# Kernel optimization log

Hardware: AMD Instinct MI355X
Metric: run time of the kernel (lower is better)

The kernel has to match this reference:

```python
import jax, jax.numpy as jnp
import numpy as np

# ---- Cl(3,0) Cayley table; blade order [1, e1,e2,e3, e12,e13,e23, e123] ----
def _build_cayley():
    blades = [0b000, 0b001, 0b010, 0b100, 0b011, 0b101, 0b110, 0b111]
    pos = {b: i for i, b in enumerate(blades)}
    def sign(a, b):
        s, a = 0, a >> 1
        while a:
            s += bin(a & b).count('1')
            a >>= 1
        return -1.0 if s & 1 else 1.0
    C = np.zeros((8, 8, 8), np.float32)
    for i, a in enumerate(blades):
        for k, b in enumerate(blades):
            C[i, pos[a ^ b], k] = sign(a, b)  # e_a * e_b -> sign * e_(a^b), metric all +1
    return jnp.asarray(C)

CAYLEY = _build_cayley()
EPS = 1e-6
SEQ = 25      # num_nodes (5) + num_edges (20)
HEADS = 8

def _expand_grades(w):
    # [..., 4] (per-grade) -> [..., 8] (per-blade), grade dims 1,3,3,1
    return jnp.concatenate([w[..., 0:1],
                            jnp.repeat(w[..., 1:2], 3, -1),
                            jnp.repeat(w[..., 2:3], 3, -1),
                            w[..., 3:4]], axis=-1)

def mv_linear(x, w, b):
    # x [N, in, 8], w [out, in, 4], b [out]; bias only on scalar blade
    y = jnp.einsum('nmi,omi->noi', x, _expand_grades(w))
    return y.at[..., 0].add(b)

def mv_layernorm(x, a):
    n = jnp.linalg.norm(x, axis=-1, keepdims=True)   # [N, c, 1] multivector norm
    n = jnp.mean(n, axis=1, keepdims=True) + EPS     # mean over channels -> [N, 1, 1]
    return a[None, :, None] * x / n

def mv_silu(x, a, b):
    # invariants: scalar component + squared grade magnitudes (mag2)
    inv = jnp.stack([x[..., 0],
                     jnp.sum(x[..., 1:4] ** 2, -1),
                     jnp.sum(x[..., 4:7] ** 2, -1),
                     x[..., 7] ** 2], axis=-1)       # [N, c, 4]
    return _expand_grades(jax.nn.sigmoid(a * inv + b)) * x

def geometric_product(a, b):
    return jnp.einsum('nci,ijk,nck->ncj', a, CAYLEY, b)


def setup_inputs() -> dict:
    key = jax.random.key(0)
    ks = iter(jax.random.split(key, 40))
    D, B = 128, 1024
    N = B * SEQ
    s = 0.05
    rn = lambda *sh: jax.random.normal(next(ks), sh, jnp.float32) * s
    return dict(
        src=jax.random.normal(next(ks), (N, D, 8), jnp.float32),
        ln1_a=jnp.ones(D, jnp.float32), ln2_a=jnp.ones(D, jnp.float32), ln3_a=jnp.ones(D, jnp.float32),
        wq=rn(D, D, 4), bq=jnp.zeros(D, jnp.float32),
        wk=rn(D, D, 4), bk=jnp.zeros(D, jnp.float32),
        wv=rn(D, D, 4), bv=jnp.zeros(D, jnp.float32),
        wo=rn(D, D, 4), bo=jnp.zeros(D, jnp.float32),
        gw1=rn(2 * D, D, 4), gb1=jnp.zeros(2 * D, jnp.float32),
        gw2=rn(2 * D, D, 4), gb2=jnp.zeros(2 * D, jnp.float32),
        gw3=rn(D, 2 * D, 4), gb3=jnp.zeros(D, jnp.float32),
        gna=jnp.ones(D, jnp.float32),
        mw1=rn(2 * D, D, 4), mb1=jnp.zeros(2 * D, jnp.float32),
        sa=jnp.ones((2 * D, 4), jnp.float32), sb=jnp.zeros((2 * D, 4), jnp.float32),
        mw2=rn(D, 2 * D, 4), mb2=jnp.zeros(D, jnp.float32),
    )


def reference(src, ln1_a, ln2_a, ln3_a, wq, bq, wk, bk, wv, bv, wo, bo,
              gw1, gb1, gw2, gb2, gw3, gb3, gna,
              mw1, mb1, sa, sb, mw2, mb2):
    N, D, _ = src.shape
    B, dh = N // SEQ, D // HEADS

    def attention(x):
        q = mv_linear(x, wq, bq).reshape(B, SEQ, HEADS, dh, 8)
        k = mv_linear(x, wk, bk).reshape(B, SEQ, HEADS, dh, 8)
        v = mv_linear(x, wv, bv).reshape(B, SEQ, HEADS, dh, 8)
        scores = jnp.einsum('bshdi,bthdi->bhst', q, k) / np.float32(np.sqrt(dh * 8))
        p = jax.nn.softmax(scores, axis=-1)
        o = jnp.einsum('bhst,bthdi->bshdi', p, v).reshape(N, D, 8)
        return mv_linear(o, wo, bo)

    # pre-norm attention + residual
    x = src + attention(mv_layernorm(src, ln1_a))
    x = mv_layernorm(x, ln2_a)
    # GP_Layer: two grade-wise linears -> geometric product -> linear -> norm
    xl = mv_linear(x, gw1, gb1)
    xr = mv_linear(x, gw2, gb2)
    g = mv_layernorm(mv_linear(geometric_product(xl, xr), gw3, gb3), gna)
    x = x + g
    x = mv_layernorm(x, ln3_a)
    # gated MLP: MVLinear -> MVSiLU -> MVLinear
    ff = mv_linear(mv_silu(mv_linear(x, mw1, mb1), sa, sb), mw2, mb2)
    return x + ff
```

## Files before the change

### kernel.cpp

```cpp
#include <hip/hip_runtime.h>
#include <hip/hip_bf16.h>
#include <math.h>

#define NROWS 25600
#define SEQL  25
#define EPSV  1e-6f

typedef __hip_bfloat16 bf16;
typedef __attribute__((ext_vector_type(4))) float f32x4;
typedef __attribute__((ext_vector_type(8))) short bf16x8;
typedef __attribute__((ext_vector_type(4))) short s16x4;
typedef unsigned int u32;

#define GLD16(gp_, lp_) __builtin_amdgcn_global_load_lds( \
    (const __attribute__((address_space(1))) u32*)(gp_), \
    (__attribute__((address_space(3))) u32*)(lp_), 16, 0, 0)

__device__ __forceinline__ float b2f(short s) {
  return __uint_as_float(((u32)(unsigned short)s) << 16);
}
__device__ __forceinline__ short f2b(float f) {
  __hip_bfloat16 h = __float2bfloat16(f);
  return *reinterpret_cast<short*>(&h);
}

__device__ __forceinline__ void gprod(const float* a, const float* b, float* r) {
  const int M[8] = {0,1,2,4,3,5,6,7};
  const int P[8] = {0,1,2,4,3,5,6,7};
#pragma unroll
  for (int i = 0; i < 8; ++i) {
    const int ma = M[i];
#pragma unroll
    for (int k = 0; k < 8; ++k) {
      const int mb = M[k];
      int par = 0;
      for (int t = ma >> 1; t; t >>= 1) par += __popc(t & mb);
      const float s = (par & 1) ? -1.f : 1.f;
      r[P[ma ^ mb]] += s * a[i] * b[k];
    }
  }
}

template<int KT, int ON>
__global__ __launch_bounds__(256) void gemm_kernel(
    const bf16* __restrict__ A, const bf16* __restrict__ W,
    const float* __restrict__ bias, const float* __restrict__ invnm,
    bf16* __restrict__ Y)
{
  __shared__ __align__(16) short As[128 * 128];
  __shared__ __align__(16) short Bs[128 * 128];
  const int tid  = threadIdx.x;
  const int lane = tid & 63;
  const int wid  = tid >> 6;
  const int pl   = blockIdx.z;
  const int g    = (pl == 0) ? 0 : ((pl < 4) ? 1 : ((pl < 7) ? 2 : 3));
  const size_t n0 = (size_t)blockIdx.x * 128;
  const int c0    = blockIdx.y * 128;
  const bf16* Ab = A + (size_t)pl * NROWS * KT + n0 * KT;
  const bf16* Wb = W + ((size_t)g * ON + c0) * KT;

  f32x4 acc[4][4];
#pragma unroll
  for (int i = 0; i < 4; ++i)
#pragma unroll
    for (int j = 0; j < 4; ++j) acc[i][j] = (f32x4){0.f, 0.f, 0.f, 0.f};

  const int wm = (wid & 1) * 64;
  const int wn = (wid >> 1) * 64;
  const int lg  = lane >> 4;
  const int c8  = lane & 15;
  const int l15 = lane & 15;

  constexpr int NC = KT / 128;
#pragma unroll
  for (int kc = 0; kc < NC; ++kc) {
#pragma unroll
    for (int j = 0; j < 8; ++j) {
      const int row = wid * 32 + j * 4 + lg;
      const int sw = (c8 ^ (row & 7)) * 8;
      const bf16* ga = Ab + (size_t)row * KT + kc * 128 + sw;
      const bf16* gb = Wb + (size_t)row * KT + kc * 128 + sw;
      GLD16(ga, &As[wid * 4096 + j * 512]);
      GLD16(gb, &Bs[wid * 4096 + j * 512]);
    }
    __syncthreads();
#pragma unroll
    for (int ks = 0; ks < 4; ++ks) {
      bf16x8 af[4], bg[4];
#pragma unroll
      for (int i = 0; i < 4; ++i) {
        const int rA = wm + i * 16 + l15;
        const int rB = wn + i * 16 + l15;
        af[i] = *(const bf16x8*)&As[rA * 128 + (((ks * 4 + lg) ^ (rA & 7)) * 8)];
        bg[i] = *(const bf16x8*)&Bs[rB * 128 + (((ks * 4 + lg) ^ (rB & 7)) * 8)];
      }
#pragma unroll
      for (int mi = 0; mi < 4; ++mi)
#pragma unroll
        for (int ni = 0; ni < 4; ++ni)
          acc[mi][ni] = __builtin_amdgcn_mfma_f32_16x16x32_bf16(af[mi], bg[ni], acc[mi][ni], 0, 0, 0);
    }
    if (kc + 1 < NC) __syncthreads();
  }

  const int cr = (lane >> 4) * 4;
  const int cc = lane & 15;
  bf16* Yb = Y + (size_t)pl * NROWS * ON;
#pragma unroll
  for (int mi = 0; mi < 4; ++mi) {
#pragma unroll
    for (int j = 0; j < 4; ++j) {
      const size_t n = n0 + wm + mi * 16 + cr + j;
      const float sc = invnm ? invnm[n] : 1.f;
#pragma unroll
      for (int ni = 0; ni < 4; ++ni) {
        const int colg = c0 + wn + ni * 16 + cc;
        float v = acc[mi][ni][j] * sc;
        if (pl == 0) v += bias[colg];
        Yb[n * ON + colg] = __float2bfloat16(v);
      }
    }
  }
}

__global__ __launch_bounds__(256) void wprep_all_kernel(
    const float* wq, const float* wk, const float* wv, const float* wo,
    const float* gw1, const float* gw2, const float* gw3,
    const float* mw1, const float* mw2,
    const float* ln1, const float* ln2, const float* ln3,
    bf16* WQ, bf16* WK, bf16* WV, bf16* WO,
    bf16* WG1, bf16* WG2, bf16* WG3, bf16* WM1, bf16* WM2)
{
  const int gid = blockIdx.x * 256 + threadIdx.x;
  const float* w; const float* ln; bf16* out; int K; int idx; int sz;
  if      (gid <  16384) { w=wq;  ln=ln1;     out=WQ;  K=128; idx=gid;          sz=16384; }
  else if (gid <  32768) { w=wk;  ln=ln1;     out=WK;  K=128; idx=gid-16384;    sz=16384; }
  else if (gid <  49152) { w=wv;  ln=ln1;     out=WV;  K=128; idx=gid-32768;    sz=16384; }
  else if (gid <  65536) { w=wo;  ln=nullptr; out=WO;  K=128; idx=gid-49152;    sz=16384; }
  else if (gid <  98304) { w=gw1; ln=ln2;     out=WG1; K=128; idx=gid-65536;    sz=32768; }
  else if (gid < 131072) { w=gw2; ln=ln2;     out=WG2; K=128; idx=gid-98304;    sz=32768; }
  else if (gid < 163840) { w=gw3; ln=nullptr; out=WG3; K=256; idx=gid-131072;   sz=32768; }
  else if (gid < 196608) { w=mw1; ln=ln3;     out=WM1; K=128; idx=gid-163840;   sz=32768; }
  else                   { w=mw2; ln=nullptr; out=WM2; K=256; idx=gid-196608;   sz=32768; }
  const int k = idx % K;
  const float s = ln ? ln[k] : 1.f;
  const float4 wv4 = *(const float4*)(w + (size_t)idx * 4);
  out[0 * sz + idx] = __float2bfloat16(wv4.x * s);
  out[1 * sz + idx] = __float2bfloat16(wv4.y * s);
  out[2 * sz + idx] = __float2bfloat16(wv4.z * s);
  out[3 * sz + idx] = __float2bfloat16(wv4.w * s);
}

__global__ __launch_bounds__(256) void repack_kernel(
    const float* __restrict__ src, bf16* __restrict__ Xp, float* __restrict__ nminv)
{
  const int tid = threadIdx.x;
  const size_t base = ((size_t)blockIdx.x * 256 + tid) * 4;
  const size_t P = (size_t)NROWS * 128;
  float v[4][8];
  const float4* sp = (const float4*)(src + base * 8);
  float part = 0.f;
#pragma unroll
  for (int e = 0; e < 4; ++e) {
    const float4 a = sp[e * 2], b = sp[e * 2 + 1];
    v[e][0]=a.x; v[e][1]=a.y; v[e][2]=a.z; v[e][3]=a.w;
    v[e][4]=b.x; v[e][5]=b.y; v[e][6]=b.z; v[e][7]=b.w;
    float ss = 0.f;
#pragma unroll
    for (int p = 0; p < 8; ++p) ss += v[e][p] * v[e][p];
    part += sqrtf(ss);
  }
#pragma unroll
  for (int p = 0; p < 8; ++p) {
    s16x4 o;
#pragma unroll
    for (int e = 0; e < 4; ++e) o[e] = f2b(v[e][p]);
    *(s16x4*)(Xp + p * P + base) = o;
  }
#pragma unroll
  for (int off = 1; off < 32; off <<= 1) part += __shfl_xor(part, off);
  if ((tid & 31) == 0) nminv[base >> 7] = 1.f / (part / 128.f + EPSV);
}

__global__ __launch_bounds__(256) void attn_kernel(
    bf16* __restrict__ Q, const bf16* __restrict__ K, const bf16* __restrict__ V)
{
  __shared__ float Pld[4][32 * 36];
  const int tid  = threadIdx.x;
  const int lane = tid & 63;
  const int wid  = tid >> 6;
  const int job  = blockIdx.x * 4 + wid;
  const int b    = job >> 3;
  const int h    = job & 7;
  const size_t PS = (size_t)NROWS * 128;
  const int rowbase = b * SEQL;
  const int l15 = lane & 15;
  const int lg  = lane >> 4;

  f32x4 acc[2][2];
#pragma unroll
  for (int si = 0; si < 2; ++si)
#pragma unroll
    for (int ti = 0; ti < 2; ++ti) acc[si][ti] = (f32x4){0.f,0.f,0.f,0.f};

#pragma unroll
  for (int ks = 0; ks < 4; ++ks) {
    const int f = ks * 32 + lg * 8;
    const int p = f >> 4, d = f & 15;
    bf16x8 aq[2], bk[2];
#pragma unroll
    for (int si = 0; si < 2; ++si) {
      int s = si * 16 + l15; if (s > 24) s = 24;
      aq[si] = *(const bf16x8*)(Q + (size_t)p * PS + (size_t)(rowbase + s) * 128 + h * 16 + d);
    }
#pragma unroll
    for (int ti = 0; ti < 2; ++ti) {
      int t = ti * 16 + l15; if (t > 24) t = 24;
      bk[ti] = *(const bf16x8*)(K + (size_t)p * PS + (size_t)(rowbase + t) * 128 + h * 16 + d);
    }
#pragma unroll
    for (int si = 0; si < 2; ++si)
#pragma unroll
      for (int ti = 0; ti < 2; ++ti)
        acc[si][ti] = __builtin_amdgcn_mfma_f32_16x16x32_bf16(aq[si], bk[ti], acc[si][ti], 0, 0, 0);
  }

  const float scale = 0.08838834764831845f;
  float pv[2][2][4];
#pragma unroll
  for (int si = 0; si < 2; ++si)
#pragma unroll
    for (int ti = 0; ti < 2; ++ti)
#pragma unroll
      for (int r = 0; r < 4; ++r) {
        float v = acc[si][ti][r] * scale;
        if (ti * 16 + l15 > 24) v = -1e30f;
        pv[si][ti][r] = v;
      }
#pragma unroll
  for (int si = 0; si < 2; ++si)
#pragma unroll
    for (int r = 0; r < 4; ++r) {
      float m = fmaxf(pv[si][0][r], pv[si][1][r]);
#pragma unroll
      for (int off = 1; off < 16; off <<= 1) m = fmaxf(m, __shfl_xor(m, off));
      const float e0 = __expf(pv[si][0][r] - m);
      const float e1 = __expf(pv[si][1][r] - m);
      float sum = e0 + e1;
#pragma unroll
      for (int off = 1; off < 16; off <<= 1) sum += __shfl_xor(sum, off);
      const float inv = 1.f / sum;
      pv[si][0][r] = e0 * inv;
      pv[si][1][r] = e1 * inv;
    }

  float* Pw = &Pld[wid][0];
#pragma unroll
  for (int si = 0; si < 2; ++si)
#pragma unroll
    for (int ti = 0; ti < 2; ++ti)
#pragma unroll
      for (int r = 0; r < 4; ++r)
        Pw[(si * 16 + lg * 4 + r) * 36 + ti * 16 + l15] = pv[si][ti][r];
  __syncthreads();

  const int p2 = lane >> 3;
  const int d2 = (lane & 7) * 2;
  const bf16* vb = V + (size_t)p2 * PS + (size_t)rowbase * 128 + h * 16 + d2;
  float vlo[32], vhi[32];
#pragma unroll
  for (int t = 0; t < SEQL; ++t) {
    const __hip_bfloat162 vv = *(const __hip_bfloat162*)(vb + (size_t)t * 128);
    vlo[t] = __bfloat162float(vv.x);
    vhi[t] = __bfloat162float(vv.y);
  }
#pragma unroll
  for (int t = SEQL; t < 32; ++t) { vlo[t] = 0.f; vhi[t] = 0.f; }

  bf16* ob = Q + (size_t)p2 * PS + (size_t)rowbase * 128 + h * 16 + d2;
  for (int s = 0; s < SEQL; ++s) {
    const float4* pr = reinterpret_cast<const float4*>(&Pld[wid][s * 36]);
    float a0 = 0.f, a1 = 0.f;
#pragma unroll
    for (int t4 = 0; t4 < 8; ++t4) {
      const float4 pq = pr[t4];
      a0 += pq.x * vlo[t4*4+0] + pq.y * vlo[t4*4+1] + pq.z * vlo[t4*4+2] + pq.w * vlo[t4*4+3];
      a1 += pq.x * vhi[t4*4+0] + pq.y * vhi[t4*4+1] + pq.z * vhi[t4*4+2] + pq.w * vhi[t4*4+3];
    }
    __hip_bfloat162 o2;
    o2.x = __float2bfloat16(a0);
    o2.y = __float2bfloat16(a1);
    *(__hip_bfloat162*)(ob + (size_t)s * 128) = o2;
  }
}

__global__ __launch_bounds__(256) void xres_kernel(
    const float* __restrict__ src, const bf16* __restrict__ AO,
    bf16* __restrict__ X, float* __restrict__ nminv)
{
  const int tid = threadIdx.x;
  const size_t base = ((size_t)blockIdx.x * 256 + tid) * 4;
  const size_t P = (size_t)NROWS * 128;
  float v[4][8];
  const float4* sp = (const float4*)(src + base * 8);
#pragma unroll
  for (int e = 0; e < 4; ++e) {
    const float4 a = sp[e * 2], b = sp[e * 2 + 1];
    v[e][0]=a.x; v[e][1]=a.y; v[e][2]=a.z; v[e][3]=a.w;
    v[e][4]=b.x; v[e][5]=b.y; v[e][6]=b.z; v[e][7]=b.w;
  }
  float part = 0.f;
  float ss[4] = {0.f, 0.f, 0.f, 0.f};
#pragma unroll
  for (int p = 0; p < 8; ++p) {
    const s16x4 av = *(const s16x4*)(AO + p * P + base);
    s16x4 o;
#pragma unroll
    for (int e = 0; e < 4; ++e) {
      v[e][p] += b2f(av[e]);
      o[e] = f2b(v[e][p]);
      ss[e] += v[e][p] * v[e][p];
    }
    *(s16x4*)(X + p * P + base) = o;
  }
#pragma unroll
  for (int e = 0; e < 4; ++e) part += sqrtf(ss[e]);
#pragma unroll
  for (int off = 1; off < 32; off <<= 1) part += __shfl_xor(part, off);
  if ((tid & 31) == 0) nminv[base >> 7] = 1.f / (part / 128.f + EPSV);
}

__global__ __launch_bounds__(256) void gp_kernel(
    bf16* __restrict__ XL, const bf16* __restrict__ XR)
{
  const size_t base = ((size_t)blockIdx.x * 256 + threadIdx.x) * 4;
  const size_t P = (size_t)NROWS * 256;
  s16x4 av[8], bv[8], rv[8];
#pragma unroll
  for (int p = 0; p < 8; ++p) {
    av[p] = *(const s16x4*)(XL + p * P + base);
    bv[p] = *(const s16x4*)(XR + p * P + base);
  }
#pragma unroll
  for (int e = 0; e < 4; ++e) {
    float a[8], b[8], r[8] = {0.f,0.f,0.f,0.f,0.f,0.f,0.f,0.f};
#pragma unroll
    for (int p = 0; p < 8; ++p) { a[p] = b2f(av[p][e]); b[p] = b2f(bv[p][e]); }
    gprod(a, b, r);
#pragma unroll
    for (int p = 0; p < 8; ++p) rv[p][e] = f2b(r[p]);
  }
#pragma unroll
  for (int p = 0; p < 8; ++p) *(s16x4*)(XL + p * P + base) = rv[p];
}

__global__ __launch_bounds__(256) void combine_kernel(
    bf16* __restrict__ X, const bf16* __restrict__ Gl,
    const float* __restrict__ ln2a, const float* __restrict__ gna,
    const float* __restrict__ nm2inv, float* __restrict__ nm4inv)
{
  const int tid = threadIdx.x;
  const size_t base = ((size_t)blockIdx.x * 256 + tid) * 4;
  const size_t P = (size_t)NROWS * 128;
  const size_t n = base >> 7;
  const int c = (int)(base & 127);

  float gv[4][8];
  float ssg[4] = {0.f,0.f,0.f,0.f};
#pragma unroll
  for (int p = 0; p < 8; ++p) {
    const s16x4 g4 = *(const s16x4*)(Gl + p * P + base);
#pragma unroll
    for (int e = 0; e < 4; ++e) { gv[e][p] = b2f(g4[e]); ssg[e] += gv[e][p] * gv[e][p]; }
  }
  float partg = sqrtf(ssg[0]) + sqrtf(ssg[1]) + sqrtf(ssg[2]) + sqrtf(ssg[3]);
#pragma unroll
  for (int off = 1; off < 32; off <<= 1) partg += __shfl_xor(partg, off);
  const float invg = 1.f / (partg / 128.f + EPSV);

  const float n2 = nm2inv[n];
  float s2[4], sg[4];
#pragma unroll
  for (int e = 0; e < 4; ++e) { s2[e] = ln2a[c + e] * n2; sg[e] = gna[c + e] * invg; }

  float ss[4] = {0.f,0.f,0.f,0.f};
#pragma unroll
  for (int p = 0; p < 8; ++p) {
    const s16x4 x4 = *(const s16x4*)(X + p * P + base);
    s16x4 o;
#pragma unroll
    for (int e = 0; e < 4; ++e) {
      const float v = s2[e] * b2f(x4[e]) + sg[e] * gv[e][p];
      o[e] = f2b(v);
      ss[e] += v * v;
    }
    *(s16x4*)(X + p * P + base) = o;
  }
  float part = sqrtf(ss[0]) + sqrtf(ss[1]) + sqrtf(ss[2]) + sqrtf(ss[3]);
#pragma unroll
  for (int off = 1; off < 32; off <<= 1) part += __shfl_xor(part, off);
  if ((tid & 31) == 0) nm4inv[n] = 1.f / (part / 128.f + EPSV);
}

__global__ __launch_bounds__(256) void silu_kernel(
    bf16* __restrict__ H, const float* __restrict__ sa, const float* __restrict__ sb)
{
  const size_t base = ((size_t)blockIdx.x * 256 + threadIdx.x) * 4;
  const int c = (int)(base & 255);
  const size_t P = (size_t)NROWS * 256;
  s16x4 hv[8];
#pragma unroll
  for (int p = 0; p < 8; ++p) hv[p] = *(const s16x4*)(H + p * P + base);
#pragma unroll
  for (int e = 0; e < 4; ++e) {
    float v[8];
#pragma unroll
    for (int p = 0; p < 8; ++p) v[p] = b2f(hv[p][e]);
    const float i0 = v[0];
    const float i1 = v[1]*v[1] + v[2]*v[2] + v[3]*v[3];
    const float i2 = v[4]*v[4] + v[5]*v[5] + v[6]*v[6];
    const float i3 = v[7]*v[7];
    const int cc = c + e;
    const float g0 = 1.f / (1.f + __expf(-(sa[cc*4+0]*i0 + sb[cc*4+0])));
    const float g1 = 1.f / (1.f + __expf(-(sa[cc*4+1]*i1 + sb[cc*4+1])));
    const float g2 = 1.f / (1.f + __expf(-(sa[cc*4+2]*i2 + sb[cc*4+2])));
    const float g3 = 1.f / (1.f + __expf(-(sa[cc*4+3]*i3 + sb[cc*4+3])));
    v[0]*=g0; v[1]*=g1; v[2]*=g1; v[3]*=g1; v[4]*=g2; v[5]*=g2; v[6]*=g2; v[7]*=g3;
#pragma unroll
    for (int p = 0; p < 8; ++p) hv[p][e] = f2b(v[p]);
  }
#pragma unroll
  for (int p = 0; p < 8; ++p) *(s16x4*)(H + p * P + base) = hv[p];
}

__global__ __launch_bounds__(256) void final_kernel(
    const bf16* __restrict__ X3, const bf16* __restrict__ FF,
    const float* __restrict__ ln3a, const float* __restrict__ nm4inv,
    float* __restrict__ out)
{
  const size_t base = ((size_t)blockIdx.x * 256 + threadIdx.x) * 4;
  const int c = (int)(base & 127);
  const size_t n = base >> 7;
  const size_t P = (size_t)NROWS * 128;
  const float nm = nm4inv[n];
  float o[4][8];
#pragma unroll
  for (int p = 0; p < 8; ++p) {
    const s16x4 x4 = *(const s16x4*)(X3 + p * P + base);
    const s16x4 f4 = *(const s16x4*)(FF + p * P + base);
#pragma unroll
    for (int e = 0; e < 4; ++e)
      o[e][p] = ln3a[c + e] * nm * b2f(x4[e]) + b2f(f4[e]);
  }
  float4* op = (float4*)(out + base * 8);
#pragma unroll
  for (int e = 0; e < 4; ++e) {
    float4 lo, hi;
    lo.x=o[e][0]; lo.y=o[e][1]; lo.z=o[e][2]; lo.w=o[e][3];
    hi.x=o[e][4]; hi.y=o[e][5]; hi.z=o[e][6]; hi.w=o[e][7];
    op[e * 2] = lo;
    op[e * 2 + 1] = hi;
  }
}

extern "C" void kernel_launch(void* const* d_in, const int* in_sizes, int n_in,
                              void* d_out, int out_size, void* d_ws, size_t ws_size,
                              hipStream_t stream) {
  (void)in_sizes; (void)n_in; (void)out_size; (void)ws_size;
  const float* src   = (const float*)d_in[0];
  const float* ln1_a = (const float*)d_in[1];
  const float* ln2_a = (const float*)d_in[2];
  const float* ln3_a = (const float*)d_in[3];
  const float* wq = (const float*)d_in[4];  const float* bq = (const float*)d_in[5];
  const float* wk = (const float*)d_in[6];  const float* bk = (const float*)d_in[7];
  const float* wv = (const float*)d_in[8];  const float* bv = (const float*)d_in[9];
  const float* wo = (const float*)d_in[10]; const float* bo = (const float*)d_in[11];
  const float* gw1 = (const float*)d_in[12]; const float* gb1 = (const float*)d_in[13];
  const float* gw2 = (const float*)d_in[14]; const float* gb2 = (const float*)d_in[15];
  const float* gw3 = (const float*)d_in[16]; const float* gb3 = (const float*)d_in[17];
  const float* gna = (const float*)d_in[18];
  const float* mw1 = (const float*)d_in[19]; const float* mb1 = (const float*)d_in[20];
  const float* sa  = (const float*)d_in[21]; const float* sb  = (const float*)d_in[22];
  const float* mw2 = (const float*)d_in[23]; const float* mb2 = (const float*)d_in[24];

  const size_t P128 = (size_t)NROWS * 128;
  char* ws = (char*)d_ws;
  bf16* R1 = (bf16*)ws;
  bf16* R2 = (bf16*)(ws + 104857600);
  bf16* WQ = (bf16*)(ws + 157286400);
  bf16* WK = WQ + 65536;
  bf16* WV = WK + 65536;
  bf16* WO = WV + 65536;
  bf16* WG1 = WO + 65536;
  bf16* WG2 = WG1 + 131072;
  bf16* WG3 = WG2 + 131072;
  bf16* WM1 = WG3 + 131072;
  bf16* WM2 = WM1 + 131072;
  float* nm1 = (float*)(ws + 159121408);
  float* nm2 = nm1 + NROWS;
  float* nm4 = nm2 + NROWS;

  bf16* Dd = (bf16*)d_out;
  bf16* Xp = R2;
  bf16* Kp = R1;
  bf16* Vp = R1 + P128;

  wprep_all_kernel<<<896, 256, 0, stream>>>(
      wq, wk, wv, wo, gw1, gw2, gw3, mw1, mw2,
      ln1_a, ln2_a, ln3_a,
      WQ, WK, WV, WO, WG1, WG2, WG3, WM1, WM2);

  repack_kernel<<<3200, 256, 0, stream>>>(src, Xp, nm1);

  dim3 g128(NROWS / 128, 1, 8), g256(NROWS / 128, 2, 8);
  gemm_kernel<128, 128><<<g128, 256, 0, stream>>>(Xp, WQ, bq, nm1, Dd);
  gemm_kernel<128, 128><<<g128, 256, 0, stream>>>(Xp, WK, bk, nm1, Kp);
  gemm_kernel<128, 128><<<g128, 256, 0, stream>>>(Xp, WV, bv, nm1, Vp);

  attn_kernel<<<2048, 256, 0, stream>>>(Dd, Kp, Vp);

  gemm_kernel<128, 128><<<g128, 256, 0, stream>>>(Dd, WO, bo, nullptr, Kp);

  xres_kernel<<<3200, 256, 0, stream>>>(src, Kp, Xp, nm2);

  gemm_kernel<128, 256><<<g256, 256, 0, stream>>>(Xp, WG1, gb1, nm2, Dd);
  gemm_kernel<128, 256><<<g256, 256, 0, stream>>>(Xp, WG2, gb2, nm2, R1);

  gp_kernel<<<6400, 256, 0, stream>>>(Dd, R1);

  gemm_kernel<256, 128><<<g128, 256, 0, stream>>>(Dd, WG3, gb3, nullptr, Kp);

  combine_kernel<<<3200, 256, 0, stream>>>(Xp, Kp, ln2_a, gna, nm2, nm4);

  gemm_kernel<128, 256><<<g256, 256, 0, stream>>>(Xp, WM1, mb1, nm4, Dd);

  silu_kernel<<<6400, 256, 0, stream>>>(Dd, sa, sb);

  gemm_kernel<256, 128><<<g128, 256, 0, stream>>>(Dd, WM2, mb2, nullptr, Vp);

  final_kernel<<<3200, 256, 0, stream>>>(Xp, Vp, ln3_a, nm4, (float*)d_out);
}
```

Before: 620.6 us.

## Merge QKV and GP GEMMs, loop blades per block, fuse final residual into last GEMM

```diff
diff --git a/kernel.cpp b/kernel.cpp
--- a/kernel.cpp
+++ b/kernel.cpp
@@ -41,83 +41,116 @@
   }
 }
 
-template<int KT, int ON>
-__global__ __launch_bounds__(256) void gemm_kernel(
-    const bf16* __restrict__ A, const bf16* __restrict__ W,
-    const float* __restrict__ bias, const float* __restrict__ invnm,
-    bf16* __restrict__ Y)
+struct GemmArgs {
+  const bf16* A; const bf16* W; const float* bias; const float* invnm;
+  bf16* Y0; bf16* Y1; bf16* Y2; bf16* Y3;
+  int yc0, yc1, yc2, yc3;
+  int ONW; int ONS;
+  const bf16* X3; const float* ln3a; const float* nm4inv; float* outf;
+};
+
+template<int KT, int KS, bool FINAL>
+__global__ __launch_bounds__(256) void gemm2_kernel(GemmArgs P)
 {
   __shared__ __align__(16) short As[128 * 128];
-  __shared__ __align__(16) short Bs[128 * 128];
   const int tid  = threadIdx.x;
   const int lane = tid & 63;
   const int wid  = tid >> 6;
-  const int pl   = blockIdx.z;
-  const int g    = (pl == 0) ? 0 : ((pl < 4) ? 1 : ((pl < 7) ? 2 : 3));
+  const int z    = blockIdx.z;
+  const int by   = blockIdx.y;
   const size_t n0 = (size_t)blockIdx.x * 128;
-  const int c0    = blockIdx.y * 128;
-  const bf16* Ab = A + (size_t)pl * NROWS * KT + n0 * KT;
-  const bf16* Wb = W + ((size_t)g * ON + c0) * KT;
-
-  f32x4 acc[4][4];
-#pragma unroll
-  for (int i = 0; i < 4; ++i)
-#pragma unroll
-    for (int j = 0; j < 4; ++j) acc[i][j] = (f32x4){0.f, 0.f, 0.f, 0.f};
-
   const int wm = (wid & 1) * 64;
   const int wn = (wid >> 1) * 64;
   const int lg  = lane >> 4;
   const int c8  = lane & 15;
   const int l15 = lane & 15;
-
   constexpr int NC = KT / 128;
-#pragma unroll
-  for (int kc = 0; kc < NC; ++kc) {
-#pragma unroll
-    for (int j = 0; j < 8; ++j) {
-      const int row = wid * 32 + j * 4 + lg;
-      const int sw = (c8 ^ (row & 7)) * 8;
-      const bf16* ga = Ab + (size_t)row * KT + kc * 128 + sw;
-      const bf16* gb = Wb + (size_t)row * KT + kc * 128 + sw;
-      GLD16(ga, &As[wid * 4096 + j * 512]);
-      GLD16(gb, &Bs[wid * 4096 + j * 512]);
-    }
-    __syncthreads();
-#pragma unroll
-    for (int ks = 0; ks < 4; ++ks) {
-      bf16x8 af[4], bg[4];
-#pragma unroll
-      for (int i = 0; i < 4; ++i) {
-        const int rA = wm + i * 16 + l15;
-        const int rB = wn + i * 16 + l15;
-        af[i] = *(const bf16x8*)&As[rA * 128 + (((ks * 4 + lg) ^ (rA & 7)) * 8)];
-        bg[i] = *(const bf16x8*)&Bs[rB * 128 + (((ks * 4 + lg) ^ (rB & 7)) * 8)];
+
+  bf16* Yb = nullptr; int yc = 0;
+  if (!FINAL) {
+    Yb = (by == 0) ? P.Y0 : (by == 1) ? P.Y1 : (by == 2) ? P.Y2 : P.Y3;
+    yc = (by == 0) ? P.yc0 : (by == 1) ? P.yc1 : (by == 2) ? P.yc2 : P.yc3;
+  }
+
+  for (int pi = 0; pi < 4; ++pi) {
+    const int p = z * 4 + pi;
+    const int g = (p == 0) ? 0 : ((p < 4) ? 1 : ((p < 7) ? 2 : 3));
+    const bf16* Ab = P.A + (size_t)p * NROWS * KS + n0 * KS;
+
+    f32x4 acc[4][4];
+#pragma unroll
+    for (int i = 0; i < 4; ++i)
+#pragma unroll
+      for (int j = 0; j < 4; ++j) acc[i][j] = (f32x4){0.f, 0.f, 0.f, 0.f};
+
+    for (int kc = 0; kc < NC; ++kc) {
+#pragma unroll
+      for (int j = 0; j < 8; ++j) {
+        const int row = wid * 32 + j * 4 + lg;
+        const int sw = (c8 ^ (row & 7)) * 8;
+        GLD16(Ab + (size_t)row * KS + kc * 128 + sw, &As[wid * 4096 + j * 512]);
       }
-#pragma unroll
-      for (int mi = 0; mi < 4; ++mi)
-#pragma unroll
-        for (int ni = 0; ni < 4; ++ni)
-          acc[mi][ni] = __builtin_amdgcn_mfma_f32_16x16x32_bf16(af[mi], bg[ni], acc[mi][ni], 0, 0, 0);
-    }
-    if (kc + 1 < NC) __syncthreads();
-  }
-
-  const int cr = (lane >> 4) * 4;
-  const int cc = lane & 15;
-  bf16* Yb = Y + (size_t)pl * NROWS * ON;
-#pragma unroll
-  for (int mi = 0; mi < 4; ++mi) {
-#pragma unroll
-    for (int j = 0; j < 4; ++j) {
-      const size_t n = n0 + wm + mi * 16 + cr + j;
-      const float sc = invnm ? invnm[n] : 1.f;
-#pragma unroll
-      for (int ni = 0; ni < 4; ++ni) {
-        const int colg = c0 + wn + ni * 16 + cc;
-        float v = acc[mi][ni][j] * sc;
-        if (pl == 0) v += bias[colg];
-        Yb[n * ON + colg] = __float2bfloat16(v);
+      bf16x8 wf[4][4];
+#pragma unroll
+      for (int ni = 0; ni < 4; ++ni)
+#pragma unroll
+        for (int ks = 0; ks < 4; ++ks)
+          wf[ni][ks] = *(const bf16x8*)(P.W +
+              ((size_t)g * P.ONW + by * 128 + wn + ni * 16 + l15) * KT +
+              kc * 128 + ks * 32 + lg * 8);
+      __syncthreads();
+#pragma unroll
+      for (int ks = 0; ks < 4; ++ks) {
+        bf16x8 af[4];
+#pragma unroll
+        for (int mi = 0; mi < 4; ++mi) {
+          const int rA = wm + mi * 16 + l15;
+          af[mi] = *(const bf16x8*)&As[rA * 128 + (((ks * 4 + lg) ^ (rA & 7)) * 8)];
+        }
+#pragma unroll
+        for (int mi = 0; mi < 4; ++mi)
+#pragma unroll
+          for (int ni = 0; ni < 4; ++ni)
+            acc[mi][ni] = __builtin_amdgcn_mfma_f32_16x16x32_bf16(af[mi], wf[ni][ks], acc[mi][ni], 0, 0, 0);
+      }
+      __syncthreads();
+    }
+
+    const int cr = (lane >> 4) * 4;
+    const int cc = lane & 15;
+    if (!FINAL) {
+      bf16* Yp = Yb + (size_t)p * NROWS * P.ONS + yc;
+#pragma unroll
+      for (int mi = 0; mi < 4; ++mi) {
+#pragma unroll
+        for (int j = 0; j < 4; ++j) {
+          const size_t n = n0 + wm + mi * 16 + cr + j;
+          const float sc = P.invnm ? P.invnm[n] : 1.f;
+#pragma unroll
+          for (int ni = 0; ni < 4; ++ni) {
+            const int cl = wn + ni * 16 + cc;
+            float v = acc[mi][ni][j] * sc;
+            if (p == 0) v += P.bias[by * 128 + cl];
+            Yp[n * P.ONS + cl] = __float2bfloat16(v);
+          }
+        }
+      }
+    } else {
+#pragma unroll
+      for (int mi = 0; mi < 4; ++mi) {
+#pragma unroll
+        for (int j = 0; j < 4; ++j) {
+          const size_t n = n0 + wm + mi * 16 + cr + j;
+          const float s3 = P.nm4inv[n];
+#pragma unroll
+          for (int ni = 0; ni < 4; ++ni) {
+            const int cl = wn + ni * 16 + cc;
+            float v = acc[mi][ni][j];
+            if (p == 0) v += P.bias[cl];
+            const float x3v = __bfloat162float(P.X3[(size_t)p * NROWS * 128 + n * 128 + cl]);
+            P.outf[(n * 128 + cl) * 8 + p] = v + P.ln3a[cl] * s3 * x3v;
+          }
+        }
       }
     }
   }
@@ -128,27 +161,40 @@
     const float* gw1, const float* gw2, const float* gw3,
     const float* mw1, const float* mw2,
     const float* ln1, const float* ln2, const float* ln3,
-    bf16* WQ, bf16* WK, bf16* WV, bf16* WO,
-    bf16* WG1, bf16* WG2, bf16* WG3, bf16* WM1, bf16* WM2)
+    bf16* WQKV, bf16* WO, bf16* WG12, bf16* WG3, bf16* WM1, bf16* WM2)
 {
   const int gid = blockIdx.x * 256 + threadIdx.x;
-  const float* w; const float* ln; bf16* out; int K; int idx; int sz;
-  if      (gid <  16384) { w=wq;  ln=ln1;     out=WQ;  K=128; idx=gid;          sz=16384; }
-  else if (gid <  32768) { w=wk;  ln=ln1;     out=WK;  K=128; idx=gid-16384;    sz=16384; }
-  else if (gid <  49152) { w=wv;  ln=ln1;     out=WV;  K=128; idx=gid-32768;    sz=16384; }
-  else if (gid <  65536) { w=wo;  ln=nullptr; out=WO;  K=128; idx=gid-49152;    sz=16384; }
-  else if (gid <  98304) { w=gw1; ln=ln2;     out=WG1; K=128; idx=gid-65536;    sz=32768; }
-  else if (gid < 131072) { w=gw2; ln=ln2;     out=WG2; K=128; idx=gid-98304;    sz=32768; }
-  else if (gid < 163840) { w=gw3; ln=nullptr; out=WG3; K=256; idx=gid-131072;   sz=32768; }
-  else if (gid < 196608) { w=mw1; ln=ln3;     out=WM1; K=128; idx=gid-163840;   sz=32768; }
-  else                   { w=mw2; ln=nullptr; out=WM2; K=256; idx=gid-196608;   sz=32768; }
+  const float* w; const float* ln; bf16* out; int K; int idx; int planeSz; int rowOfs;
+  if      (gid <  16384) { w=wq;  ln=ln1;     out=WQKV; K=128; idx=gid;        planeSz=49152; rowOfs=0;   }
+  else if (gid <  32768) { w=wk;  ln=ln1;     out=WQKV; K=128; idx=gid-16384;  planeSz=49152; rowOfs=128; }
+  else if (gid <  49152) { w=wv;  ln=ln1;     out=WQKV; K=128; idx=gid-32768;  planeSz=49152; rowOfs=256; }
+  else if (gid <  65536) { w=wo;  ln=nullptr; out=WO;   K=128; idx=gid-49152;  planeSz=16384; rowOfs=0;   }
+  else if (gid <  98304) { w=gw1; ln=ln2;     out=WG12; K=128; idx=gid-65536;  planeSz=65536; rowOfs=0;   }
+  else if (gid < 131072) { w=gw2; ln=ln2;     out=WG12; K=128; idx=gid-98304;  planeSz=65536; rowOfs=256; }
+  else if (gid < 163840) { w=gw3; ln=nullptr; out=WG3;  K=256; idx=gid-131072; planeSz=32768; rowOfs=0;   }
+  else if (gid < 196608) { w=mw1; ln=ln3;     out=WM1;  K=128; idx=gid-163840; planeSz=32768; rowOfs=0;   }
+  else                   { w=mw2; ln=nullptr; out=WM2;  K=256; idx=gid-196608; planeSz=32768; rowOfs=0;   }
   const int k = idx % K;
   const float s = ln ? ln[k] : 1.f;
   const float4 wv4 = *(const float4*)(w + (size_t)idx * 4);
-  out[0 * sz + idx] = __float2bfloat16(wv4.x * s);
-  out[1 * sz + idx] = __float2bfloat16(wv4.y * s);
-  out[2 * sz + idx] = __float2bfloat16(wv4.z * s);
-  out[3 * sz + idx] = __float2bfloat16(wv4.w * s);
+  bf16* dst = out + (size_t)rowOfs * K + idx;
+  dst[0 * planeSz] = __float2bfloat16(wv4.x * s);
+  dst[1 * planeSz] = __float2bfloat16(wv4.y * s);
+  dst[2 * planeSz] = __float2bfloat16(wv4.z * s);
+  dst[3 * planeSz] = __float2bfloat16(wv4.w * s);
+}
+
+__global__ __launch_bounds__(256) void bias_prep_kernel(
+    const float* bq, const float* bk, const float* bv,
+    const float* gb1, const float* gb2,
+    float* BQKV, float* BG12)
+{
+  const int t = blockIdx.x * 256 + threadIdx.x;
+  if      (t < 128) BQKV[t] = bq[t];
+  else if (t < 256) BQKV[t] = bk[t - 128];
+  else if (t < 384) BQKV[t] = bv[t - 256];
+  else if (t < 640) BG12[t - 384] = gb1[t - 384];
+  else if (t < 896) BG12[t - 384] = gb2[t - 640];
 }
 
 __global__ __launch_bounds__(256) void repack_kernel(
@@ -431,36 +477,6 @@
   }
 #pragma unroll
   for (int p = 0; p < 8; ++p) *(s16x4*)(H + p * P + base) = hv[p];
-}
-
-__global__ __launch_bounds__(256) void final_kernel(
-    const bf16* __restrict__ X3, const bf16* __restrict__ FF,
-    const float* __restrict__ ln3a, const float* __restrict__ nm4inv,
-    float* __restrict__ out)
-{
-  const size_t base = ((size_t)blockIdx.x * 256 + threadIdx.x) * 4;
-  const int c = (int)(base & 127);
-  const size_t n = base >> 7;
-  const size_t P = (size_t)NROWS * 128;
-  const float nm = nm4inv[n];
-  float o[4][8];
-#pragma unroll
-  for (int p = 0; p < 8; ++p) {
-    const s16x4 x4 = *(const s16x4*)(X3 + p * P + base);
-    const s16x4 f4 = *(const s16x4*)(FF + p * P + base);
-#pragma unroll
-    for (int e = 0; e < 4; ++e)
-      o[e][p] = ln3a[c + e] * nm * b2f(x4[e]) + b2f(f4[e]);
-  }
-  float4* op = (float4*)(out + base * 8);
-#pragma unroll
-  for (int e = 0; e < 4; ++e) {
-    float4 lo, hi;
-    lo.x=o[e][0]; lo.y=o[e][1]; lo.z=o[e][2]; lo.w=o[e][3];
-    hi.x=o[e][4]; hi.y=o[e][5]; hi.z=o[e][6]; hi.w=o[e][7];
-    op[e * 2] = lo;
-    op[e * 2 + 1] = hi;
-  }
 }
 
 extern "C" void kernel_launch(void* const* d_in, const int* in_sizes, int n_in,
@@ -483,60 +499,69 @@
   const float* sa  = (const float*)d_in[21]; const float* sb  = (const float*)d_in[22];
   const float* mw2 = (const float*)d_in[23]; const float* mb2 = (const float*)d_in[24];
 
-  const size_t P128 = (size_t)NROWS * 128;
   char* ws = (char*)d_ws;
-  bf16* R1 = (bf16*)ws;
-  bf16* R2 = (bf16*)(ws + 104857600);
-  bf16* WQ = (bf16*)(ws + 157286400);
-  bf16* WK = WQ + 65536;
-  bf16* WV = WK + 65536;
-  bf16* WO = WV + 65536;
-  bf16* WG1 = WO + 65536;
-  bf16* WG2 = WG1 + 131072;
-  bf16* WG3 = WG2 + 131072;
-  bf16* WM1 = WG3 + 131072;
-  bf16* WM2 = WM1 + 131072;
-  float* nm1 = (float*)(ws + 159121408);
-  float* nm2 = nm1 + NROWS;
-  float* nm4 = nm2 + NROWS;
-
-  bf16* Dd = (bf16*)d_out;
-  bf16* Xp = R2;
-  bf16* Kp = R1;
-  bf16* Vp = R1 + P128;
+  const size_t HALF = 52428800;
+
+  bf16* Xp   = (bf16*)ws;
+  bf16* Qb   = (bf16*)(ws + HALF);
+  bf16* XLH  = (bf16*)(ws + HALF);
+  bf16* WQKV = (bf16*)(ws + 157286400);
+  bf16* WO   = WQKV + 196608;
+  bf16* WG12 = WO   + 65536;
+  bf16* WG3  = WG12 + 262144;
+  bf16* WM1  = WG3  + 131072;
+  bf16* WM2  = WM1  + 131072;
+  float* BQKV = (float*)(ws + 159121408);
+  float* BG12 = BQKV + 384;
+  float* nm1  = BG12 + 512;
+  float* nm2  = nm1 + NROWS;
+  float* nm4  = nm2 + NROWS;
+
+  bf16* Kb = (bf16*)d_out;
+  bf16* Vb = (bf16*)d_out + HALF / 2;
+  bf16* AO = (bf16*)d_out;
+  bf16* XR = (bf16*)d_out;
+  bf16* Gl = (bf16*)d_out;
 
   wprep_all_kernel<<<896, 256, 0, stream>>>(
-      wq, wk, wv, wo, gw1, gw2, gw3, mw1, mw2,
-      ln1_a, ln2_a, ln3_a,
-      WQ, WK, WV, WO, WG1, WG2, WG3, WM1, WM2);
+      wq, wk, wv, wo, gw1, gw2, gw3, mw1, mw2, ln1_a, ln2_a, ln3_a,
+      WQKV, WO, WG12, WG3, WM1, WM2);
+  bias_prep_kernel<<<4, 256, 0, stream>>>(bq, bk, bv, gb1, gb2, BQKV, BG12);
 
   repack_kernel<<<3200, 256, 0, stream>>>(src, Xp, nm1);
 
-  dim3 g128(NROWS / 128, 1, 8), g256(NROWS / 128, 2, 8);
-  gemm_kernel<128, 128><<<g128, 256, 0, stream>>>(Xp, WQ, bq, nm1, Dd);
-  gemm_kernel<128, 128><<<g128, 256, 0, stream>>>(Xp, WK, bk, nm1, Kp);
-  gemm_kernel<128, 128><<<g128, 256, 0, stream>>>(Xp, WV, bv, nm1, Vp);
-
-  attn_kernel<<<2048, 256, 0, stream>>>(Dd, Kp, Vp);
-
-  gemm_kernel<128, 128><<<g128, 256, 0, stream>>>(Dd, WO, bo, nullptr, Kp);
-
-  xres_kernel<<<3200, 256, 0, stream>>>(src, Kp, Xp, nm2);
-
-  gemm_kernel<128, 256><<<g256, 256, 0, stream>>>(Xp, WG1, gb1, nm2, Dd);
-  gemm_kernel<128, 256><<<g256, 256, 0, stream>>>(Xp, WG2, gb2, nm2, R1);
-
-  gp_kernel<<<6400, 256, 0, stream>>>(Dd, R1);
-
-  gemm_kernel<256, 128><<<g128, 256, 0, stream>>>(Dd, WG3, gb3, nullptr, Kp);
-
-  combine_kernel<<<3200, 256, 0, stream>>>(Xp, Kp, ln2_a, gna, nm2, nm4);
-
-  gemm_kernel<128, 256><<<g256, 256, 0, stream>>>(Xp, WM1, mb1, nm4, Dd);
-
-  silu_kernel<<<6400, 256, 0, stream>>>(Dd, sa, sb);
-
-  gemm_kernel<256, 128><<<g128, 256, 0, stream>>>(Dd, WM2, mb2, nullptr, Vp);
-
-  final_kernel<<<3200, 256, 0, stream>>>(Xp, Vp, ln3_a, nm4, (float*)d_out);
-}
+  GemmArgs P{};
+  P = GemmArgs{Xp, WQKV, BQKV, nm1, Qb, Kb, Vb, nullptr, 0,0,0,0, 384, 128,
+               nullptr, nullptr, nullptr, nullptr};
+  gemm2_kernel<128, 128, false><<<dim3(200, 3, 2), 256, 0, stream>>>(P);
+
+  attn_kernel<<<2048, 256, 0, stream>>>(Qb, Kb, Vb);
+
+  P = GemmArgs{Qb, WO, bo, nullptr, AO, nullptr, nullptr, nullptr, 0,0,0,0, 128, 128,
+               nullptr, nullptr, nullptr, nullptr};
+  gemm2_kernel<128, 128, false><<<dim3(200, 1, 2), 256, 0, stream>>>(P);
+
+  xres_kernel<<<3200, 256, 0, stream>>>(src, AO, Xp, nm2);
+
+  P = GemmArgs{Xp, WG12, BG12, nm2, XLH, XLH, XR, XR, 0, 128, 0, 128, 512, 256,
+               nullptr, nullptr, nullptr, nullptr};
+  gemm2_kernel<128, 128, false><<<dim3(200, 4, 2), 256, 0, stream>>>(P);
+
+  gp_kernel<<<6400, 256, 0, stream>>>(XLH, XR);
+
+  P = GemmArgs{XLH, WG3, gb3, nullptr, Gl, nullptr, nullptr, nullptr, 0,0,0,0, 128, 128,
+               nullptr, nullptr, nullptr, nullptr};
+  gemm2_kernel<256, 256, false><<<dim3(200, 1, 2), 256, 0, stream>>>(P);
+
+  combine_kernel<<<3200, 256, 0, stream>>>(Xp, Gl, ln2_a, gna, nm2, nm4);
+
+  P = GemmArgs{Xp, WM1, mb1, nm4, XLH, XLH, nullptr, nullptr, 0, 128, 0, 0, 256, 256,
+               nullptr, nullptr, nullptr, nullptr};
+  gemm2_kernel<128, 128, false><<<dim3(200, 2, 2), 256, 0, stream>>>(P);
+
+  silu_kernel<<<6400, 256, 0, stream>>>(XLH, sa, sb);
+
+  P = GemmArgs{XLH, WM2, mb2, nullptr, nullptr, nullptr, nullptr, nullptr, 0,0,0,0, 128, 128,
+               Xp, ln3_a, nm4, (float*)d_out};
+  gemm2_kernel<256, 256, true><<<dim3(200, 1, 2), 256, 0, stream>>>(P);
+}
```

Result: slower. 876.0 us (+41.2%).
